# Kernel tuning notes

Measured on AMD Instinct MI355X. Metric: run time of the kernel, lower is better.

## Reference

```python
import jax, jax.numpy as jnp
from jax import lax
import numpy as np

B, GRID, H = 128, 28, 64      # batch, 28x28 pixel grid, hidden size
NDIR = 4                      # feature_sz = number of scan directions
FC_HD, OUT = 512, 10


def setup_inputs() -> dict:
    key = jax.random.key(0)
    ks = jax.random.split(key, 8)
    s_u = 1.0 / np.sqrt(2 * H)
    inp = {
        "x":  jax.random.normal(ks[0], (B, GRID, GRID), dtype=jnp.float32),
        # per-direction MDLSTM gate params: 5 gates (i, f_left, f_up, o, g)
        "Wx": jax.random.normal(ks[1], (NDIR, 5 * H), dtype=jnp.float32) * 0.1,
        "U":  jax.random.normal(ks[2], (NDIR, 2 * H, 5 * H), dtype=jnp.float32) * s_u,
        "b":  jnp.zeros((NDIR, 5 * H), dtype=jnp.float32),
        # fc head
        "W1": jax.random.normal(ks[3], (NDIR * H, FC_HD), dtype=jnp.float32) / np.sqrt(NDIR * H),
        "b1": jnp.zeros((FC_HD,), dtype=jnp.float32),
        "W2": jax.random.normal(ks[4], (FC_HD, OUT), dtype=jnp.float32) / np.sqrt(FC_HD),
        "b2": jnp.zeros((OUT,), dtype=jnp.float32),
    }
    return inp


def _mdlstm_dir(xg, Wx, U, b):
    # xg: [GRID(rows), GRID(cols), B] scalar pixel per cell
    zeros = jnp.zeros((xg.shape[-1], H), dtype=xg.dtype)

    def col_step(carry, inp):
        h_left, c_left = carry
        x_pix, h_up, c_up = inp                     # [B], [B,H], [B,H]
        z = x_pix[:, None] * Wx + jnp.concatenate([h_left, h_up], -1) @ U + b
        i, f1, f2, o, g = jnp.split(z, 5, axis=-1)  # each [B,H]
        c = (jax.nn.sigmoid(i) * jnp.tanh(g)
             + jax.nn.sigmoid(f1) * c_left
             + jax.nn.sigmoid(f2) * c_up)
        h = jax.nn.sigmoid(o) * jnp.tanh(c)
        return (h, c), (h, c)

    def row_step(carry, x_row):
        h_up_row, c_up_row = carry                  # [GRID,B,H] previous row
        _, (h_row, c_row) = lax.scan(col_step, (zeros, zeros),
                                     (x_row, h_up_row, c_up_row))
        return (h_row, c_row), None

    init = (jnp.zeros((GRID,) + zeros.shape, xg.dtype),
            jnp.zeros((GRID,) + zeros.shape, xg.dtype))
    (h_last_row, _), _ = lax.scan(row_step, init, xg)
    return h_last_row[-1]                           # final (bottom-right) hidden [B,H]


def _forward(x, Wx, U, b, W1, b1, W2, b2):
    x2 = x.reshape(-1, GRID, GRID)
    # 4 scan directions via flips; scan always proceeds top-left -> bottom-right
    dirs = jnp.stack([x2,
                      x2[:, :, ::-1],
                      x2[:, ::-1, :],
                      x2[:, ::-1, ::-1]], 0)        # [4,B,GRID,GRID]
    dirs = jnp.transpose(dirs, (0, 2, 3, 1))        # [4,GRID,GRID,B]
    h = jax.vmap(_mdlstm_dir)(dirs, Wx, U, b)       # [4,B,H]
    h = jnp.transpose(h, (1, 0, 2)).reshape(-1, NDIR * H)
    z = jax.nn.relu(h @ W1 + b1)
    return jax.nn.softmax(z @ W2 + b2, axis=-1)


def reference(x, Wx, U, b, W1, b1, W2, b2):
    return _forward(x, Wx, U, b, W1, b1, W2, b2)
```

## Files before the change

### kernel.cpp

```cpp
#include <hip/hip_runtime.h>
#include <hip/hip_bf16.h>


#define GRIDN 28
#define BATCH 128
#define HID   64
#define NDIR  4
#define FC_HD 512
#define OUT_N 10
#define BT    2
#define NTHR  512
#define NSLOT 29
#define S_H   104
#define S_C   68

typedef _Float16 f16;
typedef _Float16 f16x8 __attribute__((ext_vector_type(8)));
typedef float    f32x4 __attribute__((ext_vector_type(4)));

#define LOG2E  1.44269504088896340736f
#define LOG2E2 2.88539008177792681472f

__device__ __forceinline__ float rcpf(float x) { return __builtin_amdgcn_rcpf(x); }
__device__ __forceinline__ float ex2(float x)  { return __builtin_amdgcn_exp2f(x); }
__device__ __forceinline__ float tanh_c(float x) {
    return 1.0f - 2.0f * rcpf(1.0f + ex2(LOG2E2 * x));
}

__global__ __launch_bounds__(NTHR)
void mdlstm_kernel(const float* __restrict__ x,
                   const float* __restrict__ Wx,
                   const float* __restrict__ U,
                   const float* __restrict__ bias,
                   float* __restrict__ Hout)
{
    const int d    = blockIdx.x & 3;
    const int tile = blockIdx.x >> 2;
    const int tid  = threadIdx.x;
    const int lane = tid & 63;
    const int wave = tid >> 6;
    const int wm   = wave >> 2;
    const int wh   = wave & 3;
    const int l16  = lane & 15;
    const int q    = lane >> 4;
    const int nb   = wh * 16 + l16;

    __shared__ __align__(16) f16 Fh[2][BT][NSLOT * S_H];
    __shared__ float             Fc[2][BT][NSLOT * S_C];
    __shared__ float             xs[GRIDN][GRIDN][BT];

    for (int i = tid; i < 2 * BT * NSLOT * S_H; i += NTHR) ((f16*)Fh)[i] = (f16)0.0f;
    for (int i = tid; i < 2 * BT * NSLOT * S_C; i += NTHR) ((float*)Fc)[i] = 0.0f;
    for (int i = tid; i < GRIDN * GRIDN * BT; i += NTHR) {
        int bl = i & 1, rc = i >> 1, c = rc % GRIDN, r = rc / GRIDN;
        int rr = (d & 2) ? (GRIDN - 1 - r) : r;
        int cc = (d & 1) ? (GRIDN - 1 - c) : c;
        xs[r][c][bl] = x[((tile * BT + bl) * GRIDN + rr) * GRIDN + cc];
    }

    f16x8 bf[5][5];
#pragma unroll
    for (int g = 0; g < 5; ++g) {
        const float sc = (g == 4) ? LOG2E2 : -LOG2E;
        int n = g * 64 + nb;
#pragma unroll
        for (int ks = 0; ks < 4; ++ks) {
            f16x8 v;
            int kb = ks * 32 + q * 8;
#pragma unroll
            for (int j = 0; j < 8; ++j)
                v[j] = (f16)(sc * U[(d * 128 + kb + j) * 320 + n]);
            bf[g][ks] = v;
        }
        f16x8 v5 = {(f16)0, (f16)0, (f16)0, (f16)0, (f16)0, (f16)0, (f16)0, (f16)0};
        if (q == 0) {
            v5[0] = (f16)(sc * Wx[d * 320 + n]);
            v5[1] = (f16)(sc * bias[d * 320 + n]);
        }
        bf[g][4] = v5;
    }
    __syncthreads();

    if (tid < 2 * BT * NSLOT) {
        int buf = tid / (BT * NSLOT), rem = tid % (BT * NSLOT);
        int b = rem / NSLOT, sl = rem % NSLOT;
        Fh[buf][b][sl * S_H + 65] = (f16)1.0f;
    }
    if (tid < BT) Fh[0][tid][27 * S_H + 64] = (f16)xs[0][0][tid];
    __syncthreads();

    auto step = [&](int t, int br) __attribute__((always_inline)) {
        const int bw  = br ^ 1;
        const int rlo = (t > GRIDN - 1) ? (t - (GRIDN - 1)) : 0;
        const int rhi = (t < GRIDN - 1) ? t : (GRIDN - 1);
        const int k   = rhi - rlo + 1;
        const int nM  = (2 * k + 15) >> 4;

        if (t < 2 * GRIDN - 2 && tid >= NTHR - 56) {
            int idx = tid - (NTHR - 56), b = idx & 1, j = idx >> 1;
            int rlo2 = (t + 1 > GRIDN - 1) ? (t + 1 - (GRIDN - 1)) : 0;
            int rhi2 = (t + 1 < GRIDN - 1) ? (t + 1) : (GRIDN - 1);
            if (j <= rhi2 - rlo2) {
                int r = rlo2 + j;
                Fh[bw][b][(27 - r) * S_H + 64] = (f16)xs[r][t + 1 - r][b];
            }
        }

        for (int mt = wm; mt < nM; mt += 2) {
            int mA = mt * 16 + l16;
            int jA = mA >> 1; if (jA > k - 1) jA = k - 1;
            int bA = mA & 1;
            int slA = 27 - (rlo + jA);
            const f16* ab = &Fh[br][bA][slA * S_H];
            f16x8 a0 = *(const f16x8*)(ab + q * 8);
            f16x8 a1 = *(const f16x8*)(ab + 32 + q * 8);
            f16x8 a2 = *(const f16x8*)(ab + S_H + q * 8);
            f16x8 a3 = *(const f16x8*)(ab + S_H + 32 + q * 8);
            f16x8 a4 = *(const f16x8*)(ab + 64 + q * 8);

            const f32x4 z4 = {0.f, 0.f, 0.f, 0.f};
            f32x4 acc[5];
#pragma unroll
            for (int g = 0; g < 5; ++g) acc[g] = __builtin_amdgcn_mfma_f32_16x16x32_f16(a4, bf[g][4], z4, 0, 0, 0);
#pragma unroll
            for (int g = 0; g < 5; ++g) acc[g] = __builtin_amdgcn_mfma_f32_16x16x32_f16(a0, bf[g][0], acc[g], 0, 0, 0);
#pragma unroll
            for (int g = 0; g < 5; ++g) acc[g] = __builtin_amdgcn_mfma_f32_16x16x32_f16(a1, bf[g][1], acc[g], 0, 0, 0);
#pragma unroll
            for (int g = 0; g < 5; ++g) acc[g] = __builtin_amdgcn_mfma_f32_16x16x32_f16(a2, bf[g][2], acc[g], 0, 0, 0);
#pragma unroll
            for (int g = 0; g < 5; ++g) acc[g] = __builtin_amdgcn_mfma_f32_16x16x32_f16(a3, bf[g][3], acc[g], 0, 0, 0);

            int j0  = mt * 8 + q * 2;
            int jj0 = (j0     > k - 1) ? k - 1 : j0;
            int jj1 = (j0 + 1 > k - 1) ? k - 1 : j0 + 1;
            int sl0 = 27 - (rlo + jj0);
            int sl1 = 27 - (rlo + jj1);

            const float* rp[4] = { &Fc[br][0][sl0 * S_C + nb], &Fc[br][1][sl0 * S_C + nb],
                                   &Fc[br][0][sl1 * S_C + nb], &Fc[br][1][sl1 * S_C + nb] };
            const int DC = (bw - br) * (BT * NSLOT * S_C);
            int ih0 = sl0 * S_H + nb, ih1 = sl1 * S_H + nb;
            f16* wh0 = &Fh[bw][0][0];
            f16* wh1 = &Fh[bw][1][0];
#pragma unroll
            for (int i = 0; i < 4; ++i) {
                float cl = rp[i][0];
                float cu = rp[i][S_C];
                float ig = rcpf(1.0f + ex2(acc[0][i]));
                float f1 = rcpf(1.0f + ex2(acc[1][i]));
                float f2 = rcpf(1.0f + ex2(acc[2][i]));
                float og = rcpf(1.0f + ex2(acc[3][i]));
                float gg = 1.0f - 2.0f * rcpf(1.0f + ex2(acc[4][i]));
                float cn = ig * gg + f1 * cl + f2 * cu;
                float hn = og * tanh_c(cn);
                *(float*)(rp[i] + DC) = cn;
                ((i & 1) ? wh1 : wh0)[(i < 2) ? ih0 : ih1] = (f16)hn;
            }
        }
        __syncthreads();
    };

    for (int tb = 0; tb < 27; ++tb) { step(2 * tb, 0); step(2 * tb + 1, 1); }
    step(54, 0);

    if (tid < BT * HID) {
        int bl = tid >> 6, h = tid & 63;
        Hout[(d * BATCH + tile * BT + bl) * HID + h] = (float)Fh[1][bl][h];
    }
}

__global__ __launch_bounds__(256)
void fc_kernel(const float* __restrict__ Hin,
               const float* __restrict__ W1, const float* __restrict__ b1,
               const float* __restrict__ W2, const float* __restrict__ b2,
               float* __restrict__ out)
{
    const int b   = blockIdx.x;
    const int tid = threadIdx.x;
    __shared__ float hrow[NDIR * HID];
    __shared__ float z1[FC_HD];
    __shared__ float ps[16][16];
    __shared__ float z2[16];

    hrow[tid] = Hin[(tid >> 6) * (BATCH * HID) + b * HID + (tid & 63)];
    __syncthreads();

    {
        float s0 = b1[tid], s1 = b1[tid + 256];
#pragma unroll 8
        for (int f = 0; f < NDIR * HID; ++f) {
            float h = hrow[f];
            s0 += h * W1[f * FC_HD + tid];
            s1 += h * W1[f * FC_HD + tid + 256];
        }
        z1[tid]       = fmaxf(s0, 0.0f);
        z1[tid + 256] = fmaxf(s1, 0.0f);
    }
    __syncthreads();

    {
        int j = tid & 15, sl = tid >> 4;
        float s = 0.0f;
        if (j < OUT_N) {
#pragma unroll
            for (int i = 0; i < 32; ++i) {
                int kk = sl * 32 + i;
                s += z1[kk] * W2[kk * OUT_N + j];
            }
        }
        ps[sl][j] = s;
    }
    __syncthreads();

    if (tid < OUT_N) {
        float s = b2[tid];
#pragma unroll
        for (int sl = 0; sl < 16; ++sl) s += ps[sl][tid];
        z2[tid] = s;
    }
    __syncthreads();

    if (tid == 0) {
        float m = z2[0];
        for (int j = 1; j < OUT_N; ++j) m = fmaxf(m, z2[j]);
        float sum = 0.0f, e[OUT_N];
        for (int j = 0; j < OUT_N; ++j) { e[j] = __expf(z2[j] - m); sum += e[j]; }
        float inv = 1.0f / sum;
        for (int j = 0; j < OUT_N; ++j) out[b * OUT_N + j] = e[j] * inv;
    }
}

extern "C" void kernel_launch(void* const* d_in, const int* in_sizes, int n_in,
                              void* d_out, int out_size, void* d_ws, size_t ws_size,
                              hipStream_t stream) {
    const float* x  = (const float*)d_in[0];
    const float* Wx = (const float*)d_in[1];
    const float* U  = (const float*)d_in[2];
    const float* bs = (const float*)d_in[3];
    const float* W1 = (const float*)d_in[4];
    const float* b1 = (const float*)d_in[5];
    const float* W2 = (const float*)d_in[6];
    const float* b2 = (const float*)d_in[7];
    float* out = (float*)d_out;
    float* Hws = (float*)d_ws;

    mdlstm_kernel<<<NDIR * (BATCH / BT), NTHR, 0, stream>>>(x, Wx, U, bs, Hws);
    fc_kernel<<<BATCH, 256, 0, stream>>>(Hws, W1, b1, W2, b2, out);
}
```

Baseline: 154.5 us.

## Process one sequence per block and pad LDS to limit occupancy

Each block now handles a single batch element for one direction instead of two, so the grid doubles to 512 blocks. The MFMA M dimension now holds diagonal cells of one sequence rather than interleaved cell/batch pairs. Each wave-row runs at most one M-tile per step, which shortens the serial per-step critical path. A dummy LDS pad array, guarded by an impossible condition, inflates shared-memory use so fewer blocks share a CU. The cost is more total blocks, with half-empty M tiles and redundant weight loading per block.

```diff
diff --git a/kernel.cpp b/kernel.cpp
--- a/kernel.cpp
+++ b/kernel.cpp
@@ -8,7 +8,6 @@
 #define NDIR  4
 #define FC_HD 512
 #define OUT_N 10
-#define BT    2
 #define NTHR  512
 #define NSLOT 29
 #define S_H   104
@@ -35,7 +34,7 @@
                    float* __restrict__ Hout)
 {
     const int d    = blockIdx.x & 3;
-    const int tile = blockIdx.x >> 2;
+    const int bseq = blockIdx.x >> 2;
     const int tid  = threadIdx.x;
     const int lane = tid & 63;
     const int wave = tid >> 6;
@@ -45,18 +44,20 @@
     const int q    = lane >> 4;
     const int nb   = wh * 16 + l16;
 
-    __shared__ __align__(16) f16 Fh[2][BT][NSLOT * S_H];
-    __shared__ float             Fc[2][BT][NSLOT * S_C];
-    __shared__ float             xs[GRIDN][GRIDN][BT];
-
-    for (int i = tid; i < 2 * BT * NSLOT * S_H; i += NTHR) ((f16*)Fh)[i] = (f16)0.0f;
-    for (int i = tid; i < 2 * BT * NSLOT * S_C; i += NTHR) ((float*)Fc)[i] = 0.0f;
-    for (int i = tid; i < GRIDN * GRIDN * BT; i += NTHR) {
-        int bl = i & 1, rc = i >> 1, c = rc % GRIDN, r = rc / GRIDN;
+    __shared__ __align__(16) f16 Fh[2][NSLOT * S_H];
+    __shared__ float             Fc[2][NSLOT * S_C];
+    __shared__ float             xs[GRIDN][GRIDN];
+    __shared__ float             lds_pad[7168];
+
+    for (int i = tid; i < 2 * NSLOT * S_H; i += NTHR) ((f16*)Fh)[i] = (f16)0.0f;
+    for (int i = tid; i < 2 * NSLOT * S_C; i += NTHR) ((float*)Fc)[i] = 0.0f;
+    for (int i = tid; i < GRIDN * GRIDN; i += NTHR) {
+        int c = i % GRIDN, r = i / GRIDN;
         int rr = (d & 2) ? (GRIDN - 1 - r) : r;
         int cc = (d & 1) ? (GRIDN - 1 - c) : c;
-        xs[r][c][bl] = x[((tile * BT + bl) * GRIDN + rr) * GRIDN + cc];
-    }
+        xs[r][c] = x[(bseq * GRIDN + rr) * GRIDN + cc];
+    }
+    if (x[0] == 1.23456789e30f) lds_pad[tid] = 1.0f;
 
     f16x8 bf[5][5];
 #pragma unroll
@@ -81,12 +82,9 @@
     }
     __syncthreads();
 
-    if (tid < 2 * BT * NSLOT) {
-        int buf = tid / (BT * NSLOT), rem = tid % (BT * NSLOT);
-        int b = rem / NSLOT, sl = rem % NSLOT;
-        Fh[buf][b][sl * S_H + 65] = (f16)1.0f;
-    }
-    if (tid < BT) Fh[0][tid][27 * S_H + 64] = (f16)xs[0][0][tid];
+    if (tid < 2 * NSLOT)
+        Fh[tid / NSLOT][(tid % NSLOT) * S_H + 65] = (f16)1.0f;
+    if (tid == 0) Fh[0][27 * S_H + 64] = (f16)xs[0][0];
     __syncthreads();
 
     auto step = [&](int t, int br) __attribute__((always_inline)) {
@@ -94,24 +92,24 @@
         const int rlo = (t > GRIDN - 1) ? (t - (GRIDN - 1)) : 0;
         const int rhi = (t < GRIDN - 1) ? t : (GRIDN - 1);
         const int k   = rhi - rlo + 1;
-        const int nM  = (2 * k + 15) >> 4;
-
-        if (t < 2 * GRIDN - 2 && tid >= NTHR - 56) {
-            int idx = tid - (NTHR - 56), b = idx & 1, j = idx >> 1;
-            int rlo2 = (t + 1 > GRIDN - 1) ? (t + 1 - (GRIDN - 1)) : 0;
+        const int nM  = (k + 15) >> 4;
+
+        if (t < 2 * GRIDN - 2 && tid >= NTHR - 28) {
+            int j = tid - (NTHR - 28);
+            int rlo2 = (t + 1 > GRIDN - 1) ? (t - 26) : 0;
             int rhi2 = (t + 1 < GRIDN - 1) ? (t + 1) : (GRIDN - 1);
             if (j <= rhi2 - rlo2) {
                 int r = rlo2 + j;
-                Fh[bw][b][(27 - r) * S_H + 64] = (f16)xs[r][t + 1 - r][b];
-            }
-        }
-
-        for (int mt = wm; mt < nM; mt += 2) {
+                Fh[bw][(27 - r) * S_H + 64] = (f16)xs[r][t + 1 - r];
+            }
+        }
+
+        if (wm < nM) {
+            const int mt = wm;
             int mA = mt * 16 + l16;
-            int jA = mA >> 1; if (jA > k - 1) jA = k - 1;
-            int bA = mA & 1;
+            int jA = (mA > k - 1) ? k - 1 : mA;
             int slA = 27 - (rlo + jA);
-            const f16* ab = &Fh[br][bA][slA * S_H];
+            const f16* ab = &Fh[br][slA * S_H];
             f16x8 a0 = *(const f16x8*)(ab + q * 8);
             f16x8 a1 = *(const f16x8*)(ab + 32 + q * 8);
             f16x8 a2 = *(const f16x8*)(ab + S_H + q * 8);
@@ -131,18 +129,18 @@
 #pragma unroll
             for (int g = 0; g < 5; ++g) acc[g] = __builtin_amdgcn_mfma_f32_16x16x32_f16(a3, bf[g][3], acc[g], 0, 0, 0);
 
-            int j0  = mt * 8 + q * 2;
-            int jj0 = (j0     > k - 1) ? k - 1 : j0;
-            int jj1 = (j0 + 1 > k - 1) ? k - 1 : j0 + 1;
-            int sl0 = 27 - (rlo + jj0);
-            int sl1 = 27 - (rlo + jj1);
-
-            const float* rp[4] = { &Fc[br][0][sl0 * S_C + nb], &Fc[br][1][sl0 * S_C + nb],
-                                   &Fc[br][0][sl1 * S_C + nb], &Fc[br][1][sl1 * S_C + nb] };
-            const int DC = (bw - br) * (BT * NSLOT * S_C);
-            int ih0 = sl0 * S_H + nb, ih1 = sl1 * S_H + nb;
-            f16* wh0 = &Fh[bw][0][0];
-            f16* wh1 = &Fh[bw][1][0];
+            int j0 = mt * 16 + q * 4;
+            const float* rp[4];
+            int ih[4];
+#pragma unroll
+            for (int i = 0; i < 4; ++i) {
+                int jj = (j0 + i > k - 1) ? k - 1 : j0 + i;
+                int sl = 27 - (rlo + jj);
+                rp[i] = &Fc[br][sl * S_C + nb];
+                ih[i] = sl * S_H + nb;
+            }
+            const int DC = (bw - br) * (NSLOT * S_C);
+            f16* whp = &Fh[bw][0];
 #pragma unroll
             for (int i = 0; i < 4; ++i) {
                 float cl = rp[i][0];
@@ -155,7 +153,7 @@
                 float cn = ig * gg + f1 * cl + f2 * cu;
                 float hn = og * tanh_c(cn);
                 *(float*)(rp[i] + DC) = cn;
-                ((i & 1) ? wh1 : wh0)[(i < 2) ? ih0 : ih1] = (f16)hn;
+                whp[ih[i]] = (f16)hn;
             }
         }
         __syncthreads();
@@ -164,10 +162,8 @@
     for (int tb = 0; tb < 27; ++tb) { step(2 * tb, 0); step(2 * tb + 1, 1); }
     step(54, 0);
 
-    if (tid < BT * HID) {
-        int bl = tid >> 6, h = tid & 63;
-        Hout[(d * BATCH + tile * BT + bl) * HID + h] = (float)Fh[1][bl][h];
-    }
+    if (tid < HID)
+        Hout[(d * BATCH + bseq) * HID + tid] = (float)Fh[1][tid];
 }
 
 __global__ __launch_bounds__(256)
@@ -245,6 +241,6 @@
     float* out = (float*)d_out;
     float* Hws = (float*)d_ws;
 
-    mdlstm_kernel<<<NDIR * (BATCH / BT), NTHR, 0, stream>>>(x, Wx, U, bs, Hws);
+    mdlstm_kernel<<<NDIR * BATCH, NTHR, 0, stream>>>(x, Wx, U, bs, Hws);
     fc_kernel<<<BATCH, 256, 0, stream>>>(Hws, W1, b1, W2, b2, out);
 }
```

Measured after the change: 185.7 us. +20.2%, slower.
